# Kernel tuning notes

Hardware: AMD Instinct MI355X
Metric: run time of the kernel (lower is better)

Reference implementation:

```python
import jax, jax.numpy as jnp
import numpy as np

B, N, K = 4096, 64, 4


def _jump_sum(Ls, rho):
    # sum_k L_k @ rho @ L_k^dagger  (real dtype -> dagger == transpose)
    return jnp.einsum('kij,bjl,kml->bim', Ls, rho, Ls)


def _sandwich(U, rho):
    # U @ rho @ U^dagger
    return jnp.einsum('ij,bjl,ml->bim', U, rho, U)


def setup_inputs() -> dict:
    key = jax.random.key(0)
    k = jax.random.split(key, 6)
    eye = jnp.eye(N, dtype=jnp.float32)
    rho0 = jax.random.normal(k[0], (B, N, N), dtype=jnp.float32)
    # propagators: near-identity perturbations, Um well-conditioned for the LU solve
    U1 = eye + 0.1 * jax.random.normal(k[1], (N, N), dtype=jnp.float32)
    Um = eye + 0.1 * jax.random.normal(k[2], (N, N), dtype=jnp.float32)
    Ls0 = jax.random.normal(k[3], (K, N, N), dtype=jnp.float32)
    Lsmid = jax.random.normal(k[4], (K, N, N), dtype=jnp.float32)
    Ls1 = jax.random.normal(k[5], (K, N, N), dtype=jnp.float32)
    dt = jnp.asarray(0.01, dtype=jnp.float32)
    return {'rho0': rho0, 'U1': U1, 'Um': Um, 'Ls0': Ls0,
            'Lsmid': Lsmid, 'Ls1': Ls1, 'dt': dt}


def reference(rho0, U1, Um, Ls0, Lsmid, Ls1, dt):
    # propagator from t+dt/2 to t+dt via LU solve: solve(Um^T, U1^T)^T
    Um1 = jnp.linalg.solve(Um.T, U1.T).T

    # stage 1
    rho1 = rho0
    # stage 2 (SecondStage, no_jump_0 = Um, Ls = Ls0, aii = 0.5)
    rho2 = _sandwich(Um, rho0 + 0.5 * dt * _jump_sum(Ls0, rho1))
    # stage 3 (SameTimeStage, no_jump_0 = Um, Ls = Lsmid, aii = 0.5)
    rho3 = _sandwich(Um, rho0) + 0.5 * dt * _jump_sum(Lsmid, rho2)
    rho23 = rho2 + rho3
    # stage 4 (RKStage, no_jump_0 = U1, no_jump_i = Um1, Ls = Lsmid, aii = 1.0)
    rho4 = _sandwich(U1, rho0) + _sandwich(Um1, dt * _jump_sum(Lsmid, rho3))

    out = (_sandwich(U1, rho0 + (dt / 6) * _jump_sum(Ls0, rho1))
           + _sandwich(Um1, (dt / 3) * _jump_sum(Lsmid, rho23))
           + (dt / 6) * _jump_sum(Ls1, rho4))
    return out
```

## Files before the change

### kernel.cpp

```cpp
#include <hip/hip_runtime.h>


typedef __attribute__((ext_vector_type(16))) float f32x16;
typedef __attribute__((ext_vector_type(8))) __bf16 bf16x8;

#define MATB 8192

__device__ __forceinline__ unsigned short bf16rne(float x) {
  unsigned u = __builtin_bit_cast(unsigned, x);
  return (unsigned short)((u + 0x7FFFu + ((u >> 16) & 1u)) >> 16);
}
__device__ __forceinline__ float bflo(unsigned u) {
  return __builtin_bit_cast(float, u << 16);
}
__device__ __forceinline__ float bfhi(unsigned u) {
  return __builtin_bit_cast(float, u & 0xFFFF0000u);
}
__device__ __forceinline__ unsigned pk2(float lo, float hi) {
  return (unsigned)bf16rne(lo) | ((unsigned)bf16rne(hi) << 16);
}

union U4 { uint4 u; bf16x8 h; };

__device__ __forceinline__ bf16x8 assemble(const f32x16& t, int b8, int lh) {
  unsigned u0 = pk2(t[b8 + 0], t[b8 + 1]);
  unsigned u1 = pk2(t[b8 + 2], t[b8 + 3]);
  unsigned w0 = pk2(t[b8 + 4], t[b8 + 5]);
  unsigned w1 = pk2(t[b8 + 6], t[b8 + 7]);
  unsigned su0 = __shfl_xor(u0, 32);
  unsigned su1 = __shfl_xor(u1, 32);
  unsigned sw0 = __shfl_xor(w0, 32);
  unsigned sw1 = __shfl_xor(w1, 32);
  U4 r;
  r.u = make_uint4(lh ? sw0 : u0, lh ? sw1 : u1,
                   lh ? w0 : su0, lh ? w1 : su1);
  return r.h;
}

__device__ __forceinline__ void mm4_lg(f32x16& acc, const char* ldsP, int vp,
                                       int lh, const char* __restrict__ gQ) {
#pragma unroll
  for (int s = 0; s < 4; ++s) {
    bf16x8 a = *(const bf16x8*)(ldsP + (((2 * s + lh) ^ vp) << 4));
    bf16x8 b = *(const bf16x8*)(gQ + s * 1024);
    acc = __builtin_amdgcn_mfma_f32_32x32x16_bf16(a, b, acc, 0, 0, 0);
  }
}

__device__ __forceinline__ void secondGP(f32x16& acc, const char* __restrict__ gP,
                                         const f32x16& t0, const f32x16& t1,
                                         int lh) {
#pragma unroll
  for (int s = 0; s < 4; ++s) {
    bf16x8 q = assemble((s < 2) ? t0 : t1, (s & 1) * 8, lh);
    bf16x8 p = *(const bf16x8*)(gP + s * 1024);
    acc = __builtin_amdgcn_mfma_f32_32x32x16_bf16(p, q, acc, 0, 0, 0);
  }
}
__device__ __forceinline__ void secondGQ(f32x16& acc, const f32x16& t0,
                                         const f32x16& t1,
                                         const char* __restrict__ gQ, int lh) {
#pragma unroll
  for (int s = 0; s < 4; ++s) {
    bf16x8 p = assemble((s < 2) ? t0 : t1, (s & 1) * 8, lh);
    bf16x8 q = *(const bf16x8*)(gQ + s * 1024);
    acc = __builtin_amdgcn_mfma_f32_32x32x16_bf16(p, q, acc, 0, 0, 0);
  }
}

__device__ __forceinline__ void wtile(char* base, int ti, int slotc, int coff,
                                      int lh, const f32x16& v) {
#pragma unroll
  for (int r = 0; r < 16; ++r) {
    int row = ti * 32 + 4 * lh + (r & 3) + 8 * (r >> 2);
    int ps = (slotc ^ ((4 * ti + (r >> 2)) & 7)) << 4;
    *(unsigned short*)(base + row * 128 + ps + coff) = bf16rne(v[r]);
  }
}
__device__ __forceinline__ void wtile_rmw(char* base, int ti, int slotc, int coff,
                                          int lh, const f32x16& v, float s) {
#pragma unroll
  for (int r = 0; r < 16; ++r) {
    int row = ti * 32 + 4 * lh + (r & 3) + 8 * (r >> 2);
    int ps = (slotc ^ ((4 * ti + (r >> 2)) & 7)) << 4;
    unsigned short* p = (unsigned short*)(base + row * 128 + ps + coff);
    float old = bflo((unsigned)*p);
    *p = bf16rne(old + s * v[r]);
  }
}

__device__ __forceinline__ void axpy(char* D, const char* A, float s,
                                     const char* B, int tid) {
#pragma unroll
  for (int j = 0; j < 8; ++j) {
    int off = (tid + 256 * j) * 4;
    unsigned a = *(const unsigned*)(A + off);
    unsigned b = *(const unsigned*)(B + off);
    float lo = bflo(a) + s * bflo(b);
    float hi = bfhi(a) + s * bfhi(b);
    *(unsigned*)(D + off) = (unsigned)bf16rne(lo) | ((unsigned)bf16rne(hi) << 16);
  }
}

__global__ __launch_bounds__(256) void kraus_invert(
    const float* __restrict__ U1, const float* __restrict__ Um,
    float* __restrict__ Um1) {
  __shared__ float M[64][66];
  __shared__ float X[64][66];
  int tid = threadIdx.x;
#pragma unroll
  for (int it = 0; it < 16; ++it) {
    int idx = tid + 256 * it;
    int r = idx >> 6, c = idx & 63;
    M[r][c] = Um[idx];
    X[r][c] = (r == c) ? 1.0f : 0.0f;
  }
  __syncthreads();
  for (int k = 0; k < 64; ++k) {
    if (tid < 64) {
      float ip = 1.0f / M[k][k];
      M[k][tid] *= ip;
      X[k][tid] *= ip;
    }
    __syncthreads();
    int r = tid & 63, q = tid >> 6;
    float f = M[r][k];
    __syncthreads();
    if (r != k) {
#pragma unroll
      for (int cc = 0; cc < 16; ++cc) {
        int c = q * 16 + cc;
        M[r][c] -= f * M[k][c];
        X[r][c] -= f * X[k][c];
      }
    }
    __syncthreads();
  }
  for (int it = 0; it < 16; ++it) {
    int idx = tid + 256 * it;
    int i = idx >> 6, j = idx & 63;
    float s = 0.0f;
#pragma unroll 4
    for (int k = 0; k < 64; ++k) s += U1[i * 64 + k] * X[k][j];
    Um1[idx] = s;
  }
}

__global__ __launch_bounds__(256) void kraus_prepack(
    const float* __restrict__ U1, const float* __restrict__ Um,
    const float* __restrict__ Ls0, const float* __restrict__ Lsmid,
    const float* __restrict__ Ls1, float* __restrict__ ws) {
  const float* Um1 = ws;
  unsigned short* dst = (unsigned short*)((char*)ws + 16384);
  int o = blockIdx.x;
  const float* s;
  if (o == 0) s = U1;
  else if (o == 1) s = Um;
  else if (o == 2) s = Um1;
  else if (o < 7) s = Ls0 + (o - 3) * 4096;
  else if (o < 11) s = Lsmid + (o - 7) * 4096;
  else s = Ls1 + (o - 11) * 4096;
  unsigned short* d = dst + o * 4096;
  int tid = threadIdx.x;
#pragma unroll
  for (int j = 0; j < 16; ++j) {
    int idx = tid + 256 * j;
    int f = idx >> 9, l = (idx >> 3) & 63, i = idx & 7;
    int t = f >> 2, ss = f & 3;
    int R = t * 32 + (l & 31);
    int C = ss * 16 + (l >> 5) * 8 + i;
    d[idx] = bf16rne(s[R * 64 + C]);
  }
}

__global__ __launch_bounds__(256, 2) void kraus_main(
    const float* __restrict__ rho0g, const float* __restrict__ dtp,
    const char* __restrict__ gfrag, float* __restrict__ outg) {
  __shared__ __align__(16) char lds[4 * MATB];
  char* S0 = lds;
  char* S1 = S0 + MATB;
  char* S2 = S1 + MATB;
  char* S3 = S2 + MATB;

  const int tid = threadIdx.x;
  const int l = tid & 63, w = tid >> 6;
  const int ti = w >> 1, tj = w & 1;
  const int l31 = l & 31, lh = l >> 5;
  const int row0 = l31 * 128;
  const int row1 = (32 + l31) * 128;
  const int vk0 = l31 >> 3;
  const int vk1 = 4 + (l31 >> 3);
  const int slotc = 4 * tj + (l31 >> 3), coff = (l31 & 7) * 2;
  const float dt = dtp[0];
  const size_t b = blockIdx.x;

  auto GF = [&](int op, int blk) {
    return gfrag + op * 8192 + blk * 4096 + l * 16;
  };
  auto firsts = [&](const char* X, int op, int blk, f32x16& t0, f32x16& t1) {
    mm4_lg(t0, X + row0, vk0, lh, GF(op, blk));
    mm4_lg(t1, X + row1, vk1, lh, GF(op, blk));
  };
  auto sandPlain = [&](f32x16& acc, const char* X, int op1, int op2) {
    f32x16 t0 = {}, t1 = {};
    firsts(X, op1, ti, t0, t1);
    secondGQ(acc, t0, t1, GF(op2, tj), lh);
  };
  auto sandHat = [&](f32x16& acc, const char* X, int op1, int op2) {
    f32x16 t0 = {}, t1 = {};
    firsts(X, op1, tj, t0, t1);
    secondGP(acc, GF(op2, ti), t0, t1, lh);
  };
  auto WT = [&](char* dst, const f32x16& v) { wtile(dst, ti, slotc, coff, lh, v); };

  {
    const float* src = rho0g + b * 4096 + tid * 16;
    float vals[16];
#pragma unroll
    for (int q = 0; q < 4; ++q) {
      float4 f = *(const float4*)(src + q * 4);
      vals[q * 4 + 0] = f.x; vals[q * 4 + 1] = f.y;
      vals[q * 4 + 2] = f.z; vals[q * 4 + 3] = f.w;
    }
    int r = tid >> 2, c0 = (tid & 3) * 16;
    int sr = r >> 3, cr = (r & 7) * 2;
#pragma unroll
    for (int u = 0; u < 16; ++u) {
      int row = c0 + u;
      int ps = (sr ^ ((row >> 3) & 7)) << 4;
      *(unsigned short*)(S0 + row * 128 + ps + cr) = bf16rne(vals[u]);
    }
  }
  __syncthreads();

  f32x16 outacc = {};

  {
    f32x16 J = {};
#pragma unroll
    for (int k = 0; k < 4; ++k) sandHat(J, S0, 3 + k, 3 + k);
    WT(S1, J);
  }
  __syncthreads();

  {
    f32x16 a = {};
    sandPlain(a, S1, 0, 0);
    outacc += (dt / 6.f) * a;
    axpy(S2, S0, 0.5f * dt, S1, tid);
  }
  __syncthreads();

  {
    { f32x16 a = {}; sandPlain(a, S0, 0, 0); outacc += a; }
    { f32x16 a = {}; sandHat(a, S0, 0, 0); WT(S1, a); }
    { f32x16 a = {}; sandHat(a, S2, 1, 1); WT(S3, a); }
  }
  __syncthreads();

  {
    f32x16 a = {};
    sandHat(a, S0, 1, 1);
    WT(S2, a);
  }
  __syncthreads();

  {
    f32x16 J = {};
#pragma unroll
    for (int k = 0; k < 4; ++k) sandHat(J, S3, 7 + k, 7 + k);
    WT(S0, J);
  }
  __syncthreads();

  axpy(S3, S2, 0.5f * dt, S0, tid);
  __syncthreads();

  {
    f32x16 J = {};
#pragma unroll
    for (int k = 0; k < 4; ++k) sandHat(J, S3, 7 + k, 7 + k);
    WT(S2, J);
  }
  __syncthreads();

  {
    { f32x16 a = {}; sandPlain(a, S0, 2, 2); outacc += (dt / 3.f) * a; }
    { f32x16 a = {}; sandPlain(a, S2, 2, 2); outacc += (dt / 3.f) * a; }
    { f32x16 a = {}; sandHat(a, S2, 2, 2);
      wtile_rmw(S1, ti, slotc, coff, lh, a, dt); }
  }
  __syncthreads();

  {
    f32x16 J = {};
#pragma unroll
    for (int k = 0; k < 4; ++k) sandPlain(J, S1, 11 + k, 11 + k);
    outacc += (dt / 6.f) * J;
  }

  {
    float* op = outg + b * 4096 + (size_t)(ti * 32 + lh * 4) * 64 + tj * 32 + l31;
#pragma unroll
    for (int r = 0; r < 16; ++r) {
      int row = (r & 3) + 8 * (r >> 2);
      op[row * 64] = outacc[r];
    }
  }
}

extern "C" void kernel_launch(void* const* d_in, const int* in_sizes, int n_in,
                              void* d_out, int out_size, void* d_ws, size_t ws_size,
                              hipStream_t stream) {
  const float* rho0 = (const float*)d_in[0];
  const float* U1 = (const float*)d_in[1];
  const float* Um = (const float*)d_in[2];
  const float* Ls0 = (const float*)d_in[3];
  const float* Lsmid = (const float*)d_in[4];
  const float* Ls1 = (const float*)d_in[5];
  const float* dtp = (const float*)d_in[6];
  float* out = (float*)d_out;
  float* ws = (float*)d_ws;

  const int B = in_sizes[0] >> 12;

  kraus_invert<<<1, 256, 0, stream>>>(U1, Um, ws);
  kraus_prepack<<<15, 256, 0, stream>>>(U1, Um, Ls0, Lsmid, Ls1, ws);
  kraus_main<<<B, 256, 0, stream>>>(rho0, dtp, (const char*)d_ws + 16384, out);
}
```

Before: 283.2 us.

## Store intermediates in MFMA fragment layout and drop transposed sandwich path

Intermediate matrices in LDS are now kept directly in the MFMA operand fragment layout and written as 16-byte vector stores, replacing the per-element swizzled bf16 stores. This removes the transposed 'hat' sandwich variant: stage 2 reuses the plain U1 sandwich result for rho0, and the bf16 read-modify-write is done on packed fragments. The assemble shuffle is halved to two cross-lane exchanges, pk2 uses native bf16 conversion, and the launch bounds raise the occupancy target to 4 blocks while LDS grows to five buffers. Risks include changed register pressure at the higher occupancy target and LDS bank behaviour under the new layout.

```diff
diff --git a/kernel.cpp b/kernel.cpp
--- a/kernel.cpp
+++ b/kernel.cpp
@@ -17,7 +17,10 @@
   return __builtin_bit_cast(float, u & 0xFFFF0000u);
 }
 __device__ __forceinline__ unsigned pk2(float lo, float hi) {
-  return (unsigned)bf16rne(lo) | ((unsigned)bf16rne(hi) << 16);
+  union { __bf16 h[2]; unsigned u; } r;
+  r.h[0] = (__bf16)lo;
+  r.h[1] = (__bf16)hi;
+  return r.u;
 }
 
 union U4 { uint4 u; bf16x8 h; };
@@ -27,79 +30,14 @@
   unsigned u1 = pk2(t[b8 + 2], t[b8 + 3]);
   unsigned w0 = pk2(t[b8 + 4], t[b8 + 5]);
   unsigned w1 = pk2(t[b8 + 6], t[b8 + 7]);
-  unsigned su0 = __shfl_xor(u0, 32);
-  unsigned su1 = __shfl_xor(u1, 32);
-  unsigned sw0 = __shfl_xor(w0, 32);
-  unsigned sw1 = __shfl_xor(w1, 32);
+  unsigned z0 = lh ? u0 : w0;
+  unsigned z1 = lh ? u1 : w1;
+  unsigned r0 = __shfl_xor(z0, 32);
+  unsigned r1 = __shfl_xor(z1, 32);
   U4 r;
-  r.u = make_uint4(lh ? sw0 : u0, lh ? sw1 : u1,
-                   lh ? w0 : su0, lh ? w1 : su1);
+  r.u = make_uint4(lh ? r0 : u0, lh ? r1 : u1,
+                   lh ? w0 : r0, lh ? w1 : r1);
   return r.h;
-}
-
-__device__ __forceinline__ void mm4_lg(f32x16& acc, const char* ldsP, int vp,
-                                       int lh, const char* __restrict__ gQ) {
-#pragma unroll
-  for (int s = 0; s < 4; ++s) {
-    bf16x8 a = *(const bf16x8*)(ldsP + (((2 * s + lh) ^ vp) << 4));
-    bf16x8 b = *(const bf16x8*)(gQ + s * 1024);
-    acc = __builtin_amdgcn_mfma_f32_32x32x16_bf16(a, b, acc, 0, 0, 0);
-  }
-}
-
-__device__ __forceinline__ void secondGP(f32x16& acc, const char* __restrict__ gP,
-                                         const f32x16& t0, const f32x16& t1,
-                                         int lh) {
-#pragma unroll
-  for (int s = 0; s < 4; ++s) {
-    bf16x8 q = assemble((s < 2) ? t0 : t1, (s & 1) * 8, lh);
-    bf16x8 p = *(const bf16x8*)(gP + s * 1024);
-    acc = __builtin_amdgcn_mfma_f32_32x32x16_bf16(p, q, acc, 0, 0, 0);
-  }
-}
-__device__ __forceinline__ void secondGQ(f32x16& acc, const f32x16& t0,
-                                         const f32x16& t1,
-                                         const char* __restrict__ gQ, int lh) {
-#pragma unroll
-  for (int s = 0; s < 4; ++s) {
-    bf16x8 p = assemble((s < 2) ? t0 : t1, (s & 1) * 8, lh);
-    bf16x8 q = *(const bf16x8*)(gQ + s * 1024);
-    acc = __builtin_amdgcn_mfma_f32_32x32x16_bf16(p, q, acc, 0, 0, 0);
-  }
-}
-
-__device__ __forceinline__ void wtile(char* base, int ti, int slotc, int coff,
-                                      int lh, const f32x16& v) {
-#pragma unroll
-  for (int r = 0; r < 16; ++r) {
-    int row = ti * 32 + 4 * lh + (r & 3) + 8 * (r >> 2);
-    int ps = (slotc ^ ((4 * ti + (r >> 2)) & 7)) << 4;
-    *(unsigned short*)(base + row * 128 + ps + coff) = bf16rne(v[r]);
-  }
-}
-__device__ __forceinline__ void wtile_rmw(char* base, int ti, int slotc, int coff,
-                                          int lh, const f32x16& v, float s) {
-#pragma unroll
-  for (int r = 0; r < 16; ++r) {
-    int row = ti * 32 + 4 * lh + (r & 3) + 8 * (r >> 2);
-    int ps = (slotc ^ ((4 * ti + (r >> 2)) & 7)) << 4;
-    unsigned short* p = (unsigned short*)(base + row * 128 + ps + coff);
-    float old = bflo((unsigned)*p);
-    *p = bf16rne(old + s * v[r]);
-  }
-}
-
-__device__ __forceinline__ void axpy(char* D, const char* A, float s,
-                                     const char* B, int tid) {
-#pragma unroll
-  for (int j = 0; j < 8; ++j) {
-    int off = (tid + 256 * j) * 4;
-    unsigned a = *(const unsigned*)(A + off);
-    unsigned b = *(const unsigned*)(B + off);
-    float lo = bflo(a) + s * bflo(b);
-    float hi = bfhi(a) + s * bfhi(b);
-    *(unsigned*)(D + off) = (unsigned)bf16rne(lo) | ((unsigned)bf16rne(hi) << 16);
-  }
 }
 
 __global__ __launch_bounds__(256) void kraus_invert(
@@ -173,45 +111,64 @@
   }
 }
 
-__global__ __launch_bounds__(256, 2) void kraus_main(
+__global__ __launch_bounds__(256, 4) void kraus_main(
     const float* __restrict__ rho0g, const float* __restrict__ dtp,
     const char* __restrict__ gfrag, float* __restrict__ outg) {
-  __shared__ __align__(16) char lds[4 * MATB];
+  __shared__ __align__(16) char lds[5 * MATB];
   char* S0 = lds;
   char* S1 = S0 + MATB;
   char* S2 = S1 + MATB;
   char* S3 = S2 + MATB;
+  char* S4 = S3 + MATB;
 
   const int tid = threadIdx.x;
   const int l = tid & 63, w = tid >> 6;
   const int ti = w >> 1, tj = w & 1;
   const int l31 = l & 31, lh = l >> 5;
-  const int row0 = l31 * 128;
-  const int row1 = (32 + l31) * 128;
-  const int vk0 = l31 >> 3;
-  const int vk1 = 4 + (l31 >> 3);
-  const int slotc = 4 * tj + (l31 >> 3), coff = (l31 & 7) * 2;
+  const int fragoff = l * 16;
+  const int myslot = ((tj * 4 + 2 * ti) << 10) + fragoff;
   const float dt = dtp[0];
   const size_t b = blockIdx.x;
 
   auto GF = [&](int op, int blk) {
     return gfrag + op * 8192 + blk * 4096 + l * 16;
   };
-  auto firsts = [&](const char* X, int op, int blk, f32x16& t0, f32x16& t1) {
-    mm4_lg(t0, X + row0, vk0, lh, GF(op, blk));
-    mm4_lg(t1, X + row1, vk1, lh, GF(op, blk));
-  };
-  auto sandPlain = [&](f32x16& acc, const char* X, int op1, int op2) {
+  auto mmA = [&](f32x16& acc, const char* X, int a, const char* __restrict__ gQ) {
+#pragma unroll
+    for (int s = 0; s < 4; ++s) {
+      bf16x8 aa = *(const bf16x8*)(X + ((a * 4 + s) << 10) + fragoff);
+      bf16x8 bb = *(const bf16x8*)(gQ + s * 1024);
+      acc = __builtin_amdgcn_mfma_f32_32x32x16_bf16(aa, bb, acc, 0, 0, 0);
+    }
+  };
+  auto sandP = [&](f32x16& acc, const char* X, int op1, int op2) {
     f32x16 t0 = {}, t1 = {};
-    firsts(X, op1, ti, t0, t1);
-    secondGQ(acc, t0, t1, GF(op2, tj), lh);
-  };
-  auto sandHat = [&](f32x16& acc, const char* X, int op1, int op2) {
-    f32x16 t0 = {}, t1 = {};
-    firsts(X, op1, tj, t0, t1);
-    secondGP(acc, GF(op2, ti), t0, t1, lh);
-  };
-  auto WT = [&](char* dst, const f32x16& v) { wtile(dst, ti, slotc, coff, lh, v); };
+    mmA(t0, X, 0, GF(op1, ti));
+    mmA(t1, X, 1, GF(op1, ti));
+    const char* gQ = GF(op2, tj);
+#pragma unroll
+    for (int s = 0; s < 4; ++s) {
+      bf16x8 p = assemble((s < 2) ? t0 : t1, (s & 1) * 8, lh);
+      bf16x8 q = *(const bf16x8*)(gQ + s * 1024);
+      acc = __builtin_amdgcn_mfma_f32_32x32x16_bf16(p, q, acc, 0, 0, 0);
+    }
+  };
+  auto storeF = [&](char* dst, const f32x16& acc) {
+#pragma unroll
+    for (int sg = 0; sg < 2; ++sg) {
+      bf16x8 f = assemble(acc, sg * 8, lh);
+      *(bf16x8*)(dst + myslot + (sg << 10)) = f;
+    }
+  };
+  auto axpy = [&](char* D, const char* A, float s, const char* Bm) {
+#pragma unroll
+    for (int j = 0; j < 8; ++j) {
+      int off = (tid + 256 * j) * 4;
+      unsigned a = *(const unsigned*)(A + off);
+      unsigned bb = *(const unsigned*)(Bm + off);
+      *(unsigned*)(D + off) = pk2(bflo(a) + s * bflo(bb), bfhi(a) + s * bfhi(bb));
+    }
+  };
 
   {
     const float* src = rho0g + b * 4096 + tid * 16;
@@ -223,12 +180,12 @@
       vals[q * 4 + 2] = f.z; vals[q * 4 + 3] = f.w;
     }
     int r = tid >> 2, c0 = (tid & 3) * 16;
-    int sr = r >> 3, cr = (r & 7) * 2;
+    int base = ((r >> 4) << 10) + ((r & 7) * 2) + (((r >> 3) & 1) * 32) * 16;
 #pragma unroll
     for (int u = 0; u < 16; ++u) {
-      int row = c0 + u;
-      int ps = (sr ^ ((row >> 3) & 7)) << 4;
-      *(unsigned short*)(S0 + row * 128 + ps + cr) = bf16rne(vals[u]);
+      int c = c0 + u;
+      *(unsigned short*)(S0 + ((c >> 5) << 12) + base + (c & 31) * 16) =
+          bf16rne(vals[u]);
     }
   }
   __syncthreads();
@@ -238,64 +195,70 @@
   {
     f32x16 J = {};
 #pragma unroll
-    for (int k = 0; k < 4; ++k) sandHat(J, S0, 3 + k, 3 + k);
-    WT(S1, J);
+    for (int k = 0; k < 4; ++k) sandP(J, S0, 3 + k, 3 + k);
+    storeF(S1, J);
   }
   __syncthreads();
 
   {
     f32x16 a = {};
-    sandPlain(a, S1, 0, 0);
+    sandP(a, S1, 0, 0);
     outacc += (dt / 6.f) * a;
-    axpy(S2, S0, 0.5f * dt, S1, tid);
-  }
-  __syncthreads();
-
-  {
-    { f32x16 a = {}; sandPlain(a, S0, 0, 0); outacc += a; }
-    { f32x16 a = {}; sandHat(a, S0, 0, 0); WT(S1, a); }
-    { f32x16 a = {}; sandHat(a, S2, 1, 1); WT(S3, a); }
-  }
-  __syncthreads();
-
-  {
-    f32x16 a = {};
-    sandHat(a, S0, 1, 1);
-    WT(S2, a);
-  }
-  __syncthreads();
-
-  {
-    f32x16 J = {};
-#pragma unroll
-    for (int k = 0; k < 4; ++k) sandHat(J, S3, 7 + k, 7 + k);
-    WT(S0, J);
-  }
-  __syncthreads();
-
-  axpy(S3, S2, 0.5f * dt, S0, tid);
-  __syncthreads();
-
-  {
-    f32x16 J = {};
-#pragma unroll
-    for (int k = 0; k < 4; ++k) sandHat(J, S3, 7 + k, 7 + k);
-    WT(S2, J);
-  }
-  __syncthreads();
-
-  {
-    { f32x16 a = {}; sandPlain(a, S0, 2, 2); outacc += (dt / 3.f) * a; }
-    { f32x16 a = {}; sandPlain(a, S2, 2, 2); outacc += (dt / 3.f) * a; }
-    { f32x16 a = {}; sandHat(a, S2, 2, 2);
-      wtile_rmw(S1, ti, slotc, coff, lh, a, dt); }
-  }
-  __syncthreads();
-
-  {
-    f32x16 J = {};
-#pragma unroll
-    for (int k = 0; k < 4; ++k) sandPlain(J, S1, 11 + k, 11 + k);
+    axpy(S2, S0, 0.5f * dt, S1);
+  }
+  __syncthreads();
+
+  {
+    { f32x16 A = {}; sandP(A, S0, 0, 0); outacc += A; storeF(S1, A); }
+    { f32x16 r2 = {}; sandP(r2, S2, 1, 1); storeF(S3, r2); }
+    { f32x16 Sh = {}; sandP(Sh, S0, 1, 1); storeF(S4, Sh); }
+  }
+  __syncthreads();
+
+  {
+    f32x16 J = {};
+#pragma unroll
+    for (int k = 0; k < 4; ++k) sandP(J, S3, 7 + k, 7 + k);
+    storeF(S2, J);
+  }
+  __syncthreads();
+
+  axpy(S3, S4, 0.5f * dt, S2);
+  __syncthreads();
+
+  {
+    f32x16 J = {};
+#pragma unroll
+    for (int k = 0; k < 4; ++k) sandP(J, S3, 7 + k, 7 + k);
+    storeF(S4, J);
+  }
+  __syncthreads();
+
+  {
+    { f32x16 a = {}; sandP(a, S2, 2, 2); outacc += (dt / 3.f) * a; }
+    {
+      f32x16 g = {};
+      sandP(g, S4, 2, 2);
+      outacc += (dt / 3.f) * g;
+#pragma unroll
+      for (int sg = 0; sg < 2; ++sg) {
+        bf16x8 F = assemble(g, sg * 8, lh);
+        char* p = S1 + myslot + (sg << 10);
+        bf16x8 old = *(const bf16x8*)p;
+        bf16x8 nw;
+#pragma unroll
+        for (int i = 0; i < 8; ++i)
+          nw[i] = (__bf16)((float)old[i] + dt * (float)F[i]);
+        *(bf16x8*)p = nw;
+      }
+    }
+  }
+  __syncthreads();
+
+  {
+    f32x16 J = {};
+#pragma unroll
+    for (int k = 0; k < 4; ++k) sandP(J, S1, 11 + k, 11 + k);
     outacc += (dt / 6.f) * J;
   }
 
```

After: 284.8 us. About the same (+0.6%).
